# Optimization experiments

Hardware: AMD Instinct MI355X
Metric: run time of the kernel (lower is better)

Reference implementation:

```python
import jax, jax.numpy as jnp
import numpy as np
from jax import lax

NUM_EXPERTS = 5
K = 3


def setup_inputs() -> dict:
    key = jax.random.key(0)
    ks = jax.random.split(key, 16)
    B = 8192
    d_in, d_h = 32 * 10 * 10, 128

    def w(k, shape, fan_in):
        return jax.random.normal(k, shape, jnp.float32) / np.sqrt(fan_in)

    return {
        "x": jax.random.normal(ks[0], (B, 1, 28, 28), jnp.float32),
        # conv feature extractor: 28 -> conv5 -> 24 -> pool2 -> 12 -> conv3 -> 10
        "conv1_w": w(ks[1], (16, 1, 5, 5), 25),
        "conv1_b": jnp.zeros((16,), jnp.float32),
        "conv2_w": w(ks[2], (32, 16, 3, 3), 16 * 9),
        "conv2_b": jnp.zeros((32,), jnp.float32),
        # top-k gate
        "gate_w": w(ks[3], (d_in, NUM_EXPERTS), d_in),
        "gate_b": jnp.zeros((NUM_EXPERTS,), jnp.float32),
        # 5 experts: Linear(3200,128)-Tanh-Linear(128,128)-Tanh, stacked on axis 0
        "e1_w": w(ks[4], (NUM_EXPERTS, d_in, d_h), d_in),
        "e1_b": jnp.zeros((NUM_EXPERTS, d_h), jnp.float32),
        "e2_w": w(ks[5], (NUM_EXPERTS, d_h, d_h), d_h),
        "e2_b": jnp.zeros((NUM_EXPERTS, d_h), jnp.float32),
        # softmax head
        "sm_w": w(ks[6], (d_h, 10), d_h),
        "sm_b": jnp.zeros((10,), jnp.float32),
    }


def _conv_features(x, c1w, c1b, c2w, c2b):
    dn = ("NCHW", "OIHW", "NCHW")
    h = lax.conv_general_dilated(x, c1w, (1, 1), "VALID", dimension_numbers=dn)
    h = jax.nn.relu(h + c1b[None, :, None, None])          # [B,16,24,24]
    h = lax.reduce_window(h, -jnp.inf, lax.max, (1, 1, 2, 2), (1, 1, 2, 2), "VALID")  # [B,16,12,12]
    h = lax.conv_general_dilated(h, c2w, (1, 1), "VALID", dimension_numbers=dn)
    h = jax.nn.relu(h + c2b[None, :, None, None])          # [B,32,10,10]
    return h.reshape(h.shape[0], -1)                       # [B,3200]


def reference(x, conv1_w, conv1_b, conv2_w, conv2_b, gate_w, gate_b,
              e1_w, e1_b, e2_w, e2_b, sm_w, sm_b):
    h = _conv_features(x, conv1_w, conv1_b, conv2_w, conv2_b)  # [B, 3200]
    B = h.shape[0]

    # token-choice top-K gating over NUM_EXPERTS experts
    probs = jax.nn.softmax(h @ gate_w + gate_b, axis=-1)       # [B, E]
    topv, topi = lax.top_k(probs, K)                           # [B, K]
    topv = topv / jnp.sum(topv, axis=-1, keepdims=True)        # renormalize
    w_full = jnp.zeros((B, NUM_EXPERTS), h.dtype).at[
        jnp.arange(B)[:, None], topi].set(topv)                # [B, E] sparse combine weights

    # expert MLPs (small, computed densely and masked by gate weights)
    h1 = jnp.tanh(jnp.einsum("bd,edh->ebh", h, e1_w) + e1_b[:, None, :])   # [E,B,128]
    h2 = jnp.tanh(jnp.einsum("ebh,ehk->ebk", h1, e2_w) + e2_b[:, None, :])  # [E,B,128]
    moe_out = jnp.einsum("be,ebk->bk", w_full, h2)             # weighted sum combine, [B,128]

    logits = moe_out @ sm_w + sm_b                             # [B,10]
    return jax.nn.softmax(logits, axis=1)
```

## Files before the change

kernel.cpp:

```cpp
#include <hip/hip_runtime.h>
#include <hip/hip_bf16.h>
#include <hip/hip_fp16.h>

#define NB 8192
#define D_IN 3200
#define D_H 128
#define NE 5

typedef _Float16 f16x8 __attribute__((ext_vector_type(8)));
typedef _Float16 f16x4 __attribute__((ext_vector_type(4)));
typedef float f32x4 __attribute__((ext_vector_type(4)));

__device__ __forceinline__ void gload16(const _Float16* g, _Float16* l) {
    __builtin_amdgcn_global_load_lds(
        (const __attribute__((address_space(1))) void*)g,
        (__attribute__((address_space(3))) void*)l, 16, 0, 0);
}

__device__ __forceinline__ unsigned pack_hl(float v) {
    _Float16 vh = (_Float16)v;
    _Float16 vl = (_Float16)(v - (float)vh);
    unsigned short uh, ul;
    __builtin_memcpy(&uh, &vh, 2);
    __builtin_memcpy(&ul, &vl, 2);
    return (unsigned)uh | ((unsigned)ul << 16);
}

__global__ __launch_bounds__(256) void k_prep(const float* __restrict__ gw,
                                              const float* __restrict__ c2w,
                                              const float* __restrict__ c1w,
                                              float* __restrict__ gwC,
                                              _Float16* __restrict__ wpk,
                                              int* __restrict__ cnt) {
    int i = blockIdx.x * 256 + threadIdx.x;
    if (i < 16000) {
        int e = i / 3200, rem = i - e * 3200;
        int o = rem >> 5, co = rem & 31;
        gwC[i] = gw[(co * 100 + o) * 5 + e];
    } else if (i < 21120) {
        int j = i - 16000;
        int co = j / 160, k = j - co * 160;
        int s = k >> 4, ci = k & 15;
        float v = (s == 9) ? 0.f : c2w[(co * 16 + ci) * 9 + s];
        _Float16 vh = (_Float16)v;
        wpk[j] = vh;
        wpk[5120 + j] = (_Float16)(v - (float)vh);
    } else if (i < 21760) {
        int j = i - 21120;
        int c = (j * 1639) >> 16;
        int k = j - c * 40;
        float v = (k < 25) ? c1w[c * 25 + k] : 0.f;
        _Float16 vh = (_Float16)v;
        wpk[10240 + j] = vh;
        wpk[10880 + j] = (_Float16)(v - (float)vh);
    }
    if (blockIdx.x == 0 && threadIdx.x < NE) cnt[threadIdx.x] = 0;
}

#define PCL_S 24
__global__ __launch_bounds__(256, 4) void k_feat(
    const float* __restrict__ x, const float* __restrict__ c1b,
    const float* __restrict__ c2b,
    const float* __restrict__ gwC, const float* __restrict__ gb,
    const _Float16* __restrict__ wpk,
    const float* __restrict__ e1w, _Float16* __restrict__ wT,
    const float* __restrict__ e2w, _Float16* __restrict__ e2T,
    _Float16* __restrict__ h16, float* __restrict__ wfull)
{
    __shared__ union {
        struct {
            __align__(16) _Float16 b2h[5120];
            __align__(16) _Float16 b2l[5120];
            __align__(16) _Float16 b1h[640];
            __align__(16) _Float16 b1l[640];
            __align__(16) unsigned xs_hl[784];
            __align__(16) _Float16 pclh[144 * PCL_S];
            __align__(16) _Float16 pcll[144 * PCL_S];
            float red[32];
        } f;
        float tile[64 * 65];
    } S;
    int bid = blockIdx.x;
    int t = threadIdx.x;

    if (bid < 520) {
        if (bid < 500) {
            int e = bid / 100, rem = bid - e * 100;
            int k0 = (rem >> 1) * 64, n0 = (rem & 1) * 64;
            const float* src = e1w + (size_t)e * D_IN * D_H;
            _Float16* dst = wT + (size_t)e * D_H * D_IN;
            for (int i = 0; i < 16; ++i) {
                int idx = t + i * 256;
                int kr = idx >> 6, nc = idx & 63;
                S.tile[kr * 65 + nc] = src[(size_t)(k0 + kr) * D_H + n0 + nc];
            }
            __syncthreads();
            for (int i = 0; i < 16; ++i) {
                int idx = t + i * 256;
                int nr = idx >> 6, kc = idx & 63;
                dst[(size_t)(n0 + nr) * D_IN + k0 + kc] = (_Float16)S.tile[kc * 65 + nr];
            }
        } else {
            int idx2 = bid - 500;
            int e = idx2 >> 2, rem = idx2 & 3;
            int k0 = (rem >> 1) * 64, n0 = (rem & 1) * 64;
            const float* src = e2w + (size_t)e * D_H * D_H;
            _Float16* dst = e2T + (size_t)e * D_H * D_H;
            for (int i = 0; i < 16; ++i) {
                int idx = t + i * 256;
                int kr = idx >> 6, nc = idx & 63;
                S.tile[kr * 65 + nc] = src[(size_t)(k0 + kr) * D_H + n0 + nc];
            }
            __syncthreads();
            for (int i = 0; i < 16; ++i) {
                int idx = t + i * 256;
                int nr = idx >> 6, kc = idx & 63;
                dst[(size_t)(n0 + nr) * D_H + k0 + kc] = (_Float16)S.tile[kc * 65 + nr];
            }
        }
        return;
    }

    int b = bid - 520;
    int lane = t & 63, wv = t >> 6;
    int quad = lane >> 4, l16 = lane & 15;

    {
        _Float16* ldst = S.f.b2h;
        #pragma unroll
        for (int it = 0; it < 6; ++it) {
            int ci = t + it * 256;
            if (ci < 1440)
                gload16(wpk + ci * 8, ldst + (it * 256 + wv * 64) * 8);
        }
    }
    for (int i = t; i < 784; i += 256)
        S.f.xs_hl[i] = pack_hl(x[(size_t)b * 784 + i]);
    __syncthreads();

    {
        f16x8 b1hf = *(const f16x8*)&S.f.b1h[l16 * 40 + quad * 8];
        f16x8 b1lf = *(const f16x8*)&S.f.b1l[l16 * 40 + quad * 8];
        float bias1 = c1b[l16];
        int offw[8];
        #pragma unroll
        for (int j = 0; j < 8; ++j) {
            int k = quad * 8 + j; if (k > 24) k = 24;
            int uu = (k * 205) >> 10;
            offw[j] = k + 23 * uu;
        }
        int s_ = l16 & 3, qof = l16 >> 2;
        int dy = s_ >> 1, dx = s_ & 1;
        for (int T = wv * 9; T < wv * 9 + 9; ++T) {
            int q = T * 4 + qof;
            int qy = (q * 683) >> 13, qx = q - qy * 12;
            int base = (2 * qy + dy) * 28 + 2 * qx + dx;
            unsigned w[8];
            #pragma unroll
            for (int j = 0; j < 8; ++j) w[j] = S.f.xs_hl[base + offw[j]];
            union { f16x8 v; unsigned u[4]; } ah, al;
            #pragma unroll
            for (int jj = 0; jj < 4; ++jj) {
                ah.u[jj] = __builtin_amdgcn_perm(w[2 * jj + 1], w[2 * jj], 0x05040100u);
                al.u[jj] = __builtin_amdgcn_perm(w[2 * jj + 1], w[2 * jj], 0x07060302u);
            }
            f32x4 a1 = (f32x4){0.f, 0.f, 0.f, 0.f};
            a1 = __builtin_amdgcn_mfma_f32_16x16x32_f16(ah.v, b1hf, a1, 0, 0, 0);
            a1 = __builtin_amdgcn_mfma_f32_16x16x32_f16(ah.v, b1lf, a1, 0, 0, 0);
            a1 = __builtin_amdgcn_mfma_f32_16x16x32_f16(al.v, b1hf, a1, 0, 0, 0);
            float pv = fmaxf(fmaxf(a1[0], a1[1]), fmaxf(a1[2], a1[3]));
            pv = fmaxf(pv + bias1, 0.f);
            int pos = T * 4 + quad;
            _Float16 vh = (_Float16)pv;
            S.f.pclh[pos * PCL_S + l16] = vh;
            S.f.pcll[pos * PCL_S + l16] = (_Float16)(pv - (float)vh);
        }
    }
    __syncthreads();

    float part[5] = {0, 0, 0, 0, 0};
    int quadh = quad >> 1, quadl = quad & 1;
    const int offA[5] = {0, 2, 13, 24, 26};
    const int offB[5] = {1, 12, 14, 25, 0};
    {
        int nt = wv & 1;
        int co = nt * 16 + l16;
        f16x8 bh[5], bl[5];
        #pragma unroll
        for (int kc = 0; kc < 5; ++kc) {
            bh[kc] = *(const f16x8*)&S.f.b2h[co * 160 + kc * 32 + quad * 8];
            bl[kc] = *(const f16x8*)&S.f.b2l[co * 160 + kc * 32 + quad * 8];
        }
        float bco = c2b[co];
        for (int mt = wv >> 1; mt < 7; mt += 2) {
            int o_a = mt * 16 + l16;
            int o_cl = o_a < 100 ? o_a : 99;
            int pb = (o_cl / 10) * 12 + (o_cl % 10);
            f32x4 acc = (f32x4){0.f, 0.f, 0.f, 0.f};
            #pragma unroll
            for (int kc = 0; kc < 5; ++kc) {
                int off = quadh ? offB[kc] : offA[kc];
                f16x8 ah = *(const f16x8*)&S.f.pclh[(pb + off) * PCL_S + quadl * 8];
                f16x8 al = *(const f16x8*)&S.f.pcll[(pb + off) * PCL_S + quadl * 8];
                acc = __builtin_amdgcn_mfma_f32_16x16x32_f16(ah, bh[kc], acc, 0, 0, 0);
                acc = __builtin_amdgcn_mfma_f32_16x16x32_f16(ah, bl[kc], acc, 0, 0, 0);
                acc = __builtin_amdgcn_mfma_f32_16x16x32_f16(al, bh[kc], acc, 0, 0, 0);
            }
            if (mt < 6 || quad == 0) {
                int o0 = mt * 16 + quad * 4;
                f16x4 st;
                #pragma unroll
                for (int r = 0; r < 4; ++r) {
                    float hv = fmaxf(acc[r] + bco, 0.f);
                    st[r] = (_Float16)hv;
                    #pragma unroll
                    for (int e = 0; e < 5; ++e)
                        part[e] += hv * gwC[e * 3200 + (o0 + r) * 32 + co];
                }
                *(f16x4*)&h16[(size_t)b * D_IN + co * 100 + o0] = st;
            }
        }
    }

    #pragma unroll
    for (int e = 0; e < 5; ++e) {
        float v = part[e];
        for (int off = 32; off > 0; off >>= 1) v += __shfl_down(v, off, 64);
        if (lane == 0) S.f.red[wv * 8 + e] = v;
    }
    __syncthreads();
    if (t == 0) {
        float lg[5], p[5];
        float mx = -1e30f;
        for (int e = 0; e < 5; ++e) {
            lg[e] = S.f.red[e] + S.f.red[8 + e] + S.f.red[16 + e] + S.f.red[24 + e] + gb[e];
            mx = fmaxf(mx, lg[e]);
        }
        float sum = 0.f;
        for (int e = 0; e < 5; ++e) { p[e] = expf(lg[e] - mx); sum += p[e]; }
        for (int e = 0; e < 5; ++e) p[e] /= sum;
        bool used[5] = {false, false, false, false, false};
        float out5[5] = {0, 0, 0, 0, 0};
        int ti[3]; float tv[3]; float tsum = 0.f;
        for (int jj = 0; jj < 3; ++jj) {
            int best = 0; float bv = -1.f;
            for (int e = 0; e < 5; ++e)
                if (!used[e] && p[e] > bv) { bv = p[e]; best = e; }
            used[best] = true; ti[jj] = best; tv[jj] = bv; tsum += bv;
        }
        for (int jj = 0; jj < 3; ++jj) out5[ti[jj]] = tv[jj] / tsum;
        for (int e = 0; e < 5; ++e) wfull[b * 5 + e] = out5[e];
    }
}

__global__ __launch_bounds__(256) void k_compact(
    const float* __restrict__ wfull, int* __restrict__ cnt, int* __restrict__ lists)
{
    int tok = blockIdx.x * 256 + threadIdx.x;
    int lane = threadIdx.x & 63;
    float w[5];
    #pragma unroll
    for (int e = 0; e < 5; ++e) w[e] = wfull[(size_t)tok * 5 + e];
    #pragma unroll
    for (int e = 0; e < 5; ++e) {
        bool sel = w[e] > 0.f;
        unsigned long long mask = __ballot(sel);
        int leader = __ffsll((long long)mask) - 1;
        int base = 0;
        if (lane == leader) base = atomicAdd(&cnt[e], __popcll(mask));
        base = __shfl(base, leader, 64);
        if (sel) {
            int pos = base + __popcll(mask & ((1ull << lane) - 1ull));
            lists[e * NB + pos] = tok;
        }
    }
}

#define H1S 136
union __align__(16) SLds {
    struct { _Float16 d[12288]; } p[3];
    struct {
        __align__(16) _Float16 h1s[64 * H1S];
        __align__(16) _Float16 smwT[2048];
    } q;
};

__global__ __launch_bounds__(256, 2) void k_e1e2(
    const _Float16* __restrict__ h16, const _Float16* __restrict__ wT,
    const _Float16* __restrict__ e2T,
    const float* __restrict__ e1b, const float* __restrict__ e2b,
    const float* __restrict__ smw,
    const float* __restrict__ wfull, const int* __restrict__ cnt,
    const int* __restrict__ lists, float* __restrict__ logits)
{
    __shared__ SLds u;
    __shared__ float wfl[64];
    __shared__ int rows[64];
    int bid = blockIdx.x;
    int e = bid >> 7;
    int mt = bid & 127;
    int cnt_e = cnt[e];
    int m0 = mt * 64;
    if (m0 >= cnt_e) return;
    int t = threadIdx.x;
    int lane = t & 63, wv = t >> 6;
    int waveM = wv >> 1, waveN = wv & 1;
    int quad = lane >> 4, l16 = lane & 15;
    if (t < 64) {
        int r = m0 + t;
        int row = (r < cnt_e) ? lists[e * NB + r] : lists[e * NB];
        rows[t] = row;
        wfl[t] = (r < cnt_e) ? wfull[(size_t)row * 5 + e] : 0.f;
    }
    __syncthreads();

    const _Float16* bbase = wT + (size_t)e * (D_H * D_IN);
    int srow = t >> 2;
    int scol = (t & 3) * 8;
    const _Float16* aptr = h16 + (size_t)rows[srow] * D_IN + scol;
    const _Float16* bptr0 = bbase + (size_t)srow * D_IN + scol;
    const _Float16* bptr1 = bbase + (size_t)(64 + srow) * D_IN + scol;
    f32x4 acc[2][4];
    #pragma unroll
    for (int i = 0; i < 2; ++i)
        #pragma unroll
        for (int j = 0; j < 4; ++j) acc[i][j] = (f32x4){0.f, 0.f, 0.f, 0.f};

    _Float16* bcur = (_Float16*)&u.p[0];
    _Float16* bnxt = (_Float16*)&u.p[1];
    _Float16* bnx2 = (_Float16*)&u.p[2];
    #define STAGE(base, kk)                                           \
        do {                                                          \
            gload16(aptr  + (kk),        (base) + 0    + wv * 512);   \
            gload16(aptr  + (kk) + 32,   (base) + 2048 + wv * 512);   \
            gload16(bptr0 + (kk),        (base) + 4096 + wv * 512);   \
            gload16(bptr0 + (kk) + 32,   (base) + 8192 + wv * 512);   \
            gload16(bptr1 + (kk),        (base) + 4096 + 2048 + wv * 512); \
            gload16(bptr1 + (kk) + 32,   (base) + 8192 + 2048 + wv * 512); \
        } while (0)

    STAGE(bcur, 0);
    STAGE(bnxt, 64);
    const int NT = D_IN / 64;
    for (int it = 0; it < NT; ++it) {
        if (it + 2 < NT) {
            STAGE(bnx2, (it + 2) * 64);
            asm volatile("s_waitcnt vmcnt(12)" ::: "memory");
        } else if (it + 1 < NT) {
            asm volatile("s_waitcnt vmcnt(6)" ::: "memory");
        } else {
            asm volatile("s_waitcnt vmcnt(0)" ::: "memory");
        }
        __builtin_amdgcn_s_barrier();
        __builtin_amdgcn_sched_barrier(0);
        #pragma unroll
        for (int ch = 0; ch < 2; ++ch) {
            const _Float16* Ab = bcur + (ch ? 2048 : 0);
            const _Float16* Bb = bcur + 4096 + (ch ? 4096 : 0);
            f16x8 af[2], bf[4];
            #pragma unroll
            for (int ms = 0; ms < 2; ++ms)
                af[ms] = *(const f16x8*)&Ab[(waveM * 32 + ms * 16 + l16) * 32 + quad * 8];
            #pragma unroll
            for (int ns = 0; ns < 4; ++ns)
                bf[ns] = *(const f16x8*)&Bb[(waveN * 64 + ns * 16 + l16) * 32 + quad * 8];
            #pragma unroll
            for (int ms = 0; ms < 2; ++ms)
                #pragma unroll
                for (int ns = 0; ns < 4; ++ns)
                    acc[ms][ns] = __builtin_amdgcn_mfma_f32_16x16x32_f16(af[ms], bf[ns], acc[ms][ns], 0, 0, 0);
        }
        __builtin_amdgcn_s_barrier();
        _Float16* t0 = bcur; bcur = bnxt; bnxt = bnx2; bnx2 = t0;
    }
    #undef STAGE

    #pragma unroll
    for (int ms = 0; ms < 2; ++ms) {
        int rbase = waveM * 32 + ms * 16 + quad * 4;
        #pragma unroll
        for (int ns = 0; ns < 4; ++ns) {
            int n = waveN * 64 + ns * 16 + l16;
            float bias = e1b[e * D_H + n];
            #pragma unroll
            for (int r = 0; r < 4; ++r)
                u.q.h1s[(rbase + r) * H1S + n] = (_Float16)tanhf(acc[ms][ns][r] + bias);
        }
    }
    __syncthreads();

    const _Float16* e2g = e2T + (size_t)e * (D_H * D_H);
    f32x4 acc2[2][4];
    #pragma unroll
    for (int i = 0; i < 2; ++i)
        #pragma unroll
        for (int j = 0; j < 4; ++j) acc2[i][j] = (f32x4){0.f, 0.f, 0.f, 0.f};
    #pragma unroll
    for (int kc = 0; kc < 4; ++kc) {
        f16x8 a2[2], b2[4];
        #pragma unroll
        for (int ms = 0; ms < 2; ++ms)
            a2[ms] = *(const f16x8*)&u.q.h1s[(waveM * 32 + ms * 16 + l16) * H1S + kc * 32 + quad * 8];
        #pragma unroll
        for (int ns = 0; ns < 4; ++ns)
            b2[ns] = *(const f16x8*)&e2g[(size_t)(waveN * 64 + ns * 16 + l16) * D_H + kc * 32 + quad * 8];
        #pragma unroll
        for (int ms = 0; ms < 2; ++ms)
            #pragma unroll
            for (int ns = 0; ns < 4; ++ns)
                acc2[ms][ns] = __builtin_amdgcn_mfma_f32_16x16x32_f16(a2[ms], b2[ns], acc2[ms][ns], 0, 0, 0);
    }
    __syncthreads();

    _Float16* smwT = u.q.smwT;
    for (int i = t; i < 2048; i += 256) {
        int n = i >> 7, k = i & 127;
        smwT[i] = (_Float16)(n < 10 ? smw[k * 10 + n] : 0.f);
    }
    #pragma unroll
    for (int ms = 0; ms < 2; ++ms) {
        int rbase = waveM * 32 + ms * 16 + quad * 4;
        #pragma unroll
        for (int ns = 0; ns < 4; ++ns) {
            int n = waveN * 64 + ns * 16 + l16;
            float bias = e2b[e * D_H + n];
            #pragma unroll
            for (int r = 0; r < 4; ++r) {
                int lrow = rbase + r;
                u.q.h1s[lrow * H1S + n] = (_Float16)(wfl[lrow] * tanhf(acc2[ms][ns][r] + bias));
            }
        }
    }
    __syncthreads();

    {
        f32x4 acc3 = (f32x4){0.f, 0.f, 0.f, 0.f};
        #pragma unroll
        for (int kc = 0; kc < 4; ++kc) {
            f16x8 a3 = *(const f16x8*)&u.q.h1s[(wv * 16 + l16) * H1S + kc * 32 + quad * 8];
            f16x8 b3 = *(const f16x8*)&smwT[l16 * 128 + kc * 32 + quad * 8];
            acc3 = __builtin_amdgcn_mfma_f32_16x16x32_f16(a3, b3, acc3, 0, 0, 0);
        }
        if (l16 < 10) {
            #pragma unroll
            for (int r = 0; r < 4; ++r) {
                int row = wv * 16 + quad * 4 + r;
                unsafeAtomicAdd(&logits[(size_t)rows[row] * 10 + l16], acc3[r]);
            }
        }
    }
}

__global__ __launch_bounds__(256) void k_smax(
    const float* __restrict__ logits, const float* __restrict__ smb,
    float* __restrict__ out)
{
    int r = blockIdx.x * 256 + threadIdx.x;
    float lg[10];
    float mx = -1e30f;
    #pragma unroll
    for (int c = 0; c < 10; ++c) {
        lg[c] = logits[(size_t)r * 10 + c] + smb[c];
        mx = fmaxf(mx, lg[c]);
    }
    float s = 0.f;
    #pragma unroll
    for (int c = 0; c < 10; ++c) { lg[c] = expf(lg[c] - mx); s += lg[c]; }
    float inv = 1.f / s;
    #pragma unroll
    for (int c = 0; c < 10; ++c) out[(size_t)r * 10 + c] = lg[c] * inv;
}

extern "C" void kernel_launch(void* const* d_in, const int* in_sizes, int n_in,
                              void* d_out, int out_size, void* d_ws, size_t ws_size,
                              hipStream_t stream)
{
    const float* x   = (const float*)d_in[0];
    const float* c1w = (const float*)d_in[1];
    const float* c1b = (const float*)d_in[2];
    const float* c2w = (const float*)d_in[3];
    const float* c2b = (const float*)d_in[4];
    const float* gw  = (const float*)d_in[5];
    const float* gb  = (const float*)d_in[6];
    const float* e1w = (const float*)d_in[7];
    const float* e1b = (const float*)d_in[8];
    const float* e2w = (const float*)d_in[9];
    const float* e2b = (const float*)d_in[10];
    const float* smw = (const float*)d_in[11];
    const float* smb = (const float*)d_in[12];
    float* out = (float*)d_out;

    char* ws = (char*)d_ws;
    size_t off = 0;
    auto alloc = [&](size_t bytes) {
        void* p = ws + off;
        off += (bytes + 255) & ~(size_t)255;
        return p;
    };
    _Float16* h16 = (_Float16*)alloc((size_t)NB * D_IN * 2);
    _Float16* wT  = (_Float16*)alloc((size_t)NE * D_H * D_IN * 2);
    _Float16* e2T = (_Float16*)alloc((size_t)NE * D_H * D_H * 2);
    float* wfull  = (float*)alloc((size_t)NB * NE * 4);
    float* logits = (float*)alloc((size_t)NB * 10 * 4);
    float* gwC    = (float*)alloc((size_t)NE * D_IN * 4);
    _Float16* wpk = (_Float16*)alloc((size_t)11520 * 2);
    int* cnt      = (int*)alloc(NE * 4);
    int* lists    = (int*)alloc((size_t)NE * NB * 4);

    hipMemsetAsync(logits, 0, (size_t)NB * 10 * 4, stream);
    k_prep<<<dim3(85), 256, 0, stream>>>(gw, c2w, c1w, gwC, wpk, cnt);
    k_feat<<<dim3(520 + NB), 256, 0, stream>>>(x, c1b, c2b, gwC, gb, wpk,
                                               e1w, wT, e2w, e2T, h16, wfull);
    k_compact<<<dim3(NB / 256), 256, 0, stream>>>(wfull, cnt, lists);
    k_e1e2<<<dim3(128 * NE), 256, 0, stream>>>(h16, wT, e2T, e1b, e2b, smw,
                                               wfull, cnt, lists, logits);
    k_smax<<<dim3(NB / 256), 256, 0, stream>>>(logits, smb, out);
}
```

Before: 251.8 us.

## Replace sparse expert token compaction with dense per-expert tiles and grouped block order

Drops the compaction kernel and the gathered token lists. Every expert now runs over all tokens in contiguous 64-row tiles, with rows whose gate weight is zero contributing nothing. Block indices are remapped so each group of 8 row tiles is processed by all 5 experts together, so the same h16 rows are reused across experts in cache. This removes a launch, the atomics and the indirect row gathers, but raises expert GEMM work from 3/5 of tokens to all tokens.

```diff
diff --git a/kernel.cpp b/kernel.cpp
--- a/kernel.cpp
+++ b/kernel.cpp
@@ -30,8 +30,7 @@
                                               const float* __restrict__ c2w,
                                               const float* __restrict__ c1w,
                                               float* __restrict__ gwC,
-                                              _Float16* __restrict__ wpk,
-                                              int* __restrict__ cnt) {
+                                              _Float16* __restrict__ wpk) {
     int i = blockIdx.x * 256 + threadIdx.x;
     if (i < 16000) {
         int e = i / 3200, rem = i - e * 3200;
@@ -54,7 +53,6 @@
         wpk[10240 + j] = vh;
         wpk[10880 + j] = (_Float16)(v - (float)vh);
     }
-    if (blockIdx.x == 0 && threadIdx.x < NE) cnt[threadIdx.x] = 0;
 }
 
 #define PCL_S 24
@@ -253,29 +251,6 @@
     }
 }
 
-__global__ __launch_bounds__(256) void k_compact(
-    const float* __restrict__ wfull, int* __restrict__ cnt, int* __restrict__ lists)
-{
-    int tok = blockIdx.x * 256 + threadIdx.x;
-    int lane = threadIdx.x & 63;
-    float w[5];
-    #pragma unroll
-    for (int e = 0; e < 5; ++e) w[e] = wfull[(size_t)tok * 5 + e];
-    #pragma unroll
-    for (int e = 0; e < 5; ++e) {
-        bool sel = w[e] > 0.f;
-        unsigned long long mask = __ballot(sel);
-        int leader = __ffsll((long long)mask) - 1;
-        int base = 0;
-        if (lane == leader) base = atomicAdd(&cnt[e], __popcll(mask));
-        base = __shfl(base, leader, 64);
-        if (sel) {
-            int pos = base + __popcll(mask & ((1ull << lane) - 1ull));
-            lists[e * NB + pos] = tok;
-        }
-    }
-}
-
 #define H1S 136
 union __align__(16) SLds {
     struct { _Float16 d[12288]; } p[3];
@@ -290,34 +265,26 @@
     const _Float16* __restrict__ e2T,
     const float* __restrict__ e1b, const float* __restrict__ e2b,
     const float* __restrict__ smw,
-    const float* __restrict__ wfull, const int* __restrict__ cnt,
-    const int* __restrict__ lists, float* __restrict__ logits)
+    const float* __restrict__ wfull, float* __restrict__ logits)
 {
     __shared__ SLds u;
     __shared__ float wfl[64];
-    __shared__ int rows[64];
     int bid = blockIdx.x;
-    int e = bid >> 7;
-    int mt = bid & 127;
-    int cnt_e = cnt[e];
+    int g = bid / 40, rr0 = bid - g * 40;
+    int e = rr0 >> 3, xi = rr0 & 7;
+    int mt = g * 8 + xi;
     int m0 = mt * 64;
-    if (m0 >= cnt_e) return;
     int t = threadIdx.x;
     int lane = t & 63, wv = t >> 6;
     int waveM = wv >> 1, waveN = wv & 1;
     int quad = lane >> 4, l16 = lane & 15;
-    if (t < 64) {
-        int r = m0 + t;
-        int row = (r < cnt_e) ? lists[e * NB + r] : lists[e * NB];
-        rows[t] = row;
-        wfl[t] = (r < cnt_e) ? wfull[(size_t)row * 5 + e] : 0.f;
-    }
+    if (t < 64) wfl[t] = wfull[(size_t)(m0 + t) * 5 + e];
     __syncthreads();
 
     const _Float16* bbase = wT + (size_t)e * (D_H * D_IN);
     int srow = t >> 2;
     int scol = (t & 3) * 8;
-    const _Float16* aptr = h16 + (size_t)rows[srow] * D_IN + scol;
+    const _Float16* aptr = h16 + (size_t)(m0 + srow) * D_IN + scol;
     const _Float16* bptr0 = bbase + (size_t)srow * D_IN + scol;
     const _Float16* bptr1 = bbase + (size_t)(64 + srow) * D_IN + scol;
     f32x4 acc[2][4];
@@ -445,7 +412,7 @@
             #pragma unroll
             for (int r = 0; r < 4; ++r) {
                 int row = wv * 16 + quad * 4 + r;
-                unsafeAtomicAdd(&logits[(size_t)rows[row] * 10 + l16], acc3[r]);
+                unsafeAtomicAdd(&logits[(size_t)(m0 + row) * 10 + l16], acc3[r]);
             }
         }
     }
@@ -504,15 +471,12 @@
     float* logits = (float*)alloc((size_t)NB * 10 * 4);
     float* gwC    = (float*)alloc((size_t)NE * D_IN * 4);
     _Float16* wpk = (_Float16*)alloc((size_t)11520 * 2);
-    int* cnt      = (int*)alloc(NE * 4);
-    int* lists    = (int*)alloc((size_t)NE * NB * 4);
 
     hipMemsetAsync(logits, 0, (size_t)NB * 10 * 4, stream);
-    k_prep<<<dim3(85), 256, 0, stream>>>(gw, c2w, c1w, gwC, wpk, cnt);
+    k_prep<<<dim3(85), 256, 0, stream>>>(gw, c2w, c1w, gwC, wpk);
     k_feat<<<dim3(520 + NB), 256, 0, stream>>>(x, c1b, c2b, gwC, gb, wpk,
                                                e1w, wT, e2w, e2T, h16, wfull);
-    k_compact<<<dim3(NB / 256), 256, 0, stream>>>(wfull, cnt, lists);
     k_e1e2<<<dim3(128 * NE), 256, 0, stream>>>(h16, wT, e2T, e1b, e2b, smw,
-                                               wfull, cnt, lists, logits);
+                                               wfull, logits);
     k_smax<<<dim3(NB / 256), 256, 0, stream>>>(logits, smb, out);
 }
```

After: 281.4 us. +11.8%, slower.
